# Kernel tuning notes

Measured on AMD Instinct MI355X. Metric: run time of the kernel, lower is better.

Reference implementation:

```python
import jax, jax.numpy as jnp
import numpy as np

N_NODES = 100000


def gcn_conv(x, edge_index, edge_weight, W, b):
    """PyG GCNConv: out = D^-1/2 (A + I) D^-1/2 X W + b (self-loop weight 1)."""
    n = x.shape[0]
    src, dst = edge_index[0], edge_index[1]
    loop = jnp.arange(n)
    src_sl = jnp.concatenate([src, loop])
    dst_sl = jnp.concatenate([dst, loop])
    ew_sl = jnp.concatenate([edge_weight, jnp.ones((n,), x.dtype)])
    deg = jax.ops.segment_sum(ew_sl, dst_sl, num_segments=n)  # [N]
    dinv = jnp.where(deg > 0, jax.lax.rsqrt(deg), 0.0)
    norm = dinv[src_sl] * ew_sl * dinv[dst_sl]  # [E+N]
    h = x @ W  # [N, out_dim] dense transform before propagation
    msg = h[src_sl] * norm[:, None]  # gather + scale, [E+N, out_dim]
    out = jax.ops.segment_sum(msg, dst_sl, num_segments=n)  # scatter-add
    return out + b


def setup_inputs() -> dict:
    key = jax.random.key(0)
    ks = jax.random.split(key, 9)
    in_dim, hidden, latent = 128, 64, 32
    n, e = N_NODES, 1600000
    x = jax.random.normal(ks[0], (n, in_dim), dtype=jnp.float32)
    edge_index = jax.random.randint(ks[1], (2, e), 0, n, dtype=jnp.int64)
    edge_weight = jax.random.uniform(ks[2], (e,), dtype=jnp.float32)
    def glorot(k, fan_in, fan_out):
        s = jnp.sqrt(6.0 / (fan_in + fan_out))
        return jax.random.uniform(k, (fan_in, fan_out), jnp.float32, -s, s)
    return {
        "x": x,
        "edge_index": edge_index,
        "edge_weight": edge_weight,
        "W1": glorot(ks[3], in_dim, hidden),
        "b1": jnp.zeros((hidden,), jnp.float32),
        "W_mu": glorot(ks[4], hidden, latent),
        "b_mu": jnp.zeros((latent,), jnp.float32),
        "W_lv": glorot(ks[5], hidden, latent),
        "b_lv": jnp.zeros((latent,), jnp.float32),
    }


def reference(x, edge_index, edge_weight, W1, b1, W_mu, b_mu, W_lv, b_lv):
    h = jax.nn.relu(gcn_conv(x, edge_index, edge_weight, W1, b1))
    mu = gcn_conv(h, edge_index, edge_weight, W_mu, b_mu)
    logvar = gcn_conv(h, edge_index, edge_weight, W_lv, b_lv)
    return (mu, logvar)
```

## Files before the change

### kernel.cpp

```cpp
#include <hip/hip_runtime.h>

static __device__ __forceinline__ float4 ld4(const float* p) { return *(const float4*)p; }
static __device__ __forceinline__ float b2f(unsigned short u) {
    return __uint_as_float((unsigned)u << 16);
}
static __device__ __forceinline__ float b2f_lo(unsigned u) { return __uint_as_float(u << 16); }
static __device__ __forceinline__ float b2f_hi(unsigned u) { return __uint_as_float(u & 0xFFFF0000u); }
static __device__ __forceinline__ unsigned short f2b(float f) {
    unsigned x = __float_as_uint(f);
    return (unsigned short)((x + 0x7FFFu + ((x >> 16) & 1u)) >> 16);
}
static __device__ __forceinline__ unsigned pk2(float lo, float hi) {
    return (unsigned)f2b(lo) | ((unsigned)f2b(hi) << 16);
}

#define NPB 256
#define CAPE 5120


__global__ __launch_bounds__(256) void k_fused1(const float* __restrict__ A,
                                                const float* __restrict__ W0,
                                                const float* __restrict__ dinv_unused,
                                                unsigned short* __restrict__ gout,
                                                const int* __restrict__ src,
                                                const int* __restrict__ dst,
                                                const float* __restrict__ ew,
                                                int* __restrict__ bin_cnt,
                                                unsigned long long* __restrict__ ebuf,
                                                int n, int E, int gb, int NB) {
    __shared__ float Ws[64 * 64];
    __shared__ float Xs[64 * 64];
    __shared__ int hist[512];
    __shared__ int hbase[512];
    int tid = threadIdx.x;

    if ((int)blockIdx.x < gb) {
        int row0 = blockIdx.x * 64;
        int c0 = (tid & 15) * 4;
        int r0 = (tid >> 4) * 4;
        float4 acc[4] = {};
        #pragma unroll
        for (int p = 0; p < 2; p++) {
            for (int j = tid; j < 1024; j += 256)
                *(float4*)&Ws[j * 4] = ld4(W0 + p * 4096 + j * 4);
            for (int j = tid; j < 1024; j += 256) {
                int r = j >> 4, kc = j & 15;
                int grow = row0 + r;
                float4 v = make_float4(0.f, 0.f, 0.f, 0.f);
                if (grow < n) v = ld4(A + (size_t)grow * 128 + p * 64 + kc * 4);
                *(float4*)&Xs[r * 64 + kc * 4] = v;
            }
            __syncthreads();
            #pragma unroll 4
            for (int kk = 0; kk < 64; kk += 4) {
                float4 w0 = ld4(&Ws[(kk + 0) * 64 + c0]);
                float4 w1 = ld4(&Ws[(kk + 1) * 64 + c0]);
                float4 w2 = ld4(&Ws[(kk + 2) * 64 + c0]);
                float4 w3 = ld4(&Ws[(kk + 3) * 64 + c0]);
                #pragma unroll
                for (int i = 0; i < 4; i++) {
                    float4 a = ld4(&Xs[(r0 + i) * 64 + kk]);
                    acc[i].x = fmaf(a.x, w0.x, fmaf(a.y, w1.x, fmaf(a.z, w2.x, fmaf(a.w, w3.x, acc[i].x))));
                    acc[i].y = fmaf(a.x, w0.y, fmaf(a.y, w1.y, fmaf(a.z, w2.y, fmaf(a.w, w3.y, acc[i].y))));
                    acc[i].z = fmaf(a.x, w0.z, fmaf(a.y, w1.z, fmaf(a.z, w2.z, fmaf(a.w, w3.z, acc[i].z))));
                    acc[i].w = fmaf(a.x, w0.w, fmaf(a.y, w1.w, fmaf(a.z, w2.w, fmaf(a.w, w3.w, acc[i].w))));
                }
            }
            __syncthreads();
        }
        #pragma unroll
        for (int i = 0; i < 4; i++) {
            int grow = row0 + r0 + i;
            if (grow < n) {
                ushort4 u = make_ushort4(f2b(acc[i].x), f2b(acc[i].y), f2b(acc[i].z), f2b(acc[i].w));
                *(ushort4*)&gout[(size_t)grow * 64 + c0] = u;
            }
        }
    } else {
        for (int j = tid; j < NB; j += 256) hist[j] = 0;
        __syncthreads();
        int e0 = ((int)blockIdx.x - gb) * 4096;
        unsigned long long pk[16]; int bb[16]; int loc[16];
        #pragma unroll
        for (int j = 0; j < 16; j++) {
            int e = e0 + j * 256 + tid;
            if (e < E) {
                int s = src[e];
                int d = dst[e];
                float w = ew[e];
                bb[j] = d >> 8;
                pk[j] = ((unsigned long long)__float_as_uint(w) << 32) |
                        (unsigned)((d & (NPB - 1)) << 17) | (unsigned)s;
                loc[j] = atomicAdd(&hist[bb[j]], 1);
            } else bb[j] = -1;
        }
        __syncthreads();
        for (int j = tid; j < NB; j += 256) hbase[j] = atomicAdd(&bin_cnt[j], hist[j]);
        __syncthreads();
        #pragma unroll
        for (int j = 0; j < 16; j++) {
            if (bb[j] >= 0)
                ebuf[(size_t)bb[j] * CAPE + hbase[bb[j]] + loc[j]] = pk[j];
        }
    }
}

__global__ __launch_bounds__(512) void k_csr_build(const unsigned long long* __restrict__ ebuf,
                                                   const int* __restrict__ bin_cnt,
                                                   int2* __restrict__ rowcnt,
                                                   float* __restrict__ dinv,
                                                   unsigned long long* __restrict__ csr,
                                                   int n) {
    __shared__ unsigned long long eL[CAPE];
    __shared__ unsigned cntL[NPB];
    __shared__ unsigned ewsL[NPB];
    __shared__ unsigned fillL[NPB];
    __shared__ int scanL[512];
    __shared__ int rowL[NPB];
    __shared__ int binbase_s;
    int b = blockIdx.x;
    int tid = threadIdx.x;
    if (tid < NPB) { cntL[tid] = 0; ewsL[tid] = 0; fillL[tid] = 0; }
    scanL[tid] = (tid < b) ? bin_cnt[tid] : 0;
    __syncthreads();
    int m = bin_cnt[b];
    const unsigned long long* eb = ebuf + (size_t)b * CAPE;
    for (int i = tid; i < m; i += 512) {
        unsigned long long pk = eb[i];
        eL[i] = pk;
        int ld = (int)((pk >> 17) & (NPB - 1));
        float w = __uint_as_float((unsigned)(pk >> 32));
        atomicAdd(&cntL[ld], 1u);
        atomicAdd(&ewsL[ld], (unsigned)(w * 16777216.0f));
    }
    __syncthreads();
    #pragma unroll
    for (int off = 256; off > 0; off >>= 1) {
        if (tid < off) scanL[tid] += scanL[tid + off];
        __syncthreads();
    }
    if (tid == 0) binbase_s = scanL[0];
    __syncthreads();
    int v = (tid < NPB) ? (int)cntL[tid] : 0;
    scanL[tid] = v;
    __syncthreads();
    #pragma unroll
    for (int off = 1; off < 512; off <<= 1) {
        int t = (tid >= off) ? scanL[tid - off] : 0;
        __syncthreads();
        scanL[tid] += t;
        __syncthreads();
    }
    if (tid < NPB) {
        int rp = binbase_s + scanL[tid] - v;
        rowL[tid] = rp;
        int node = b * NPB + tid;
        if (node < n) {
            rowcnt[node] = make_int2(rp, v);
            dinv[node] = rsqrtf(1.0f + (float)ewsL[tid] * (1.0f / 16777216.0f));
        }
    }
    __syncthreads();
    for (int i = tid; i < m; i += 512) {
        unsigned long long pk = eL[i];
        int s = (int)(pk & 0x1FFFF);
        int ld = (int)((pk >> 17) & (NPB - 1));
        int pos = rowL[ld] + (int)atomicAdd(&fillL[ld], 1u);
        csr[pos] = (unsigned long long)(unsigned)s | (pk & 0xFFFFFFFF00000000ull);
    }
}

__global__ __launch_bounds__(256) void k_scale(unsigned short* __restrict__ h0,
                                               const float* __restrict__ dinv, int n) {
    int i = blockIdx.x * 256 + threadIdx.x;
    if (i >= n * 16) return;
    int node = i >> 4;
    float sc = dinv[node];
    ushort4 u = *(ushort4*)&h0[(size_t)i * 4];
    u = make_ushort4(f2b(b2f(u.x) * sc), f2b(b2f(u.y) * sc),
                     f2b(b2f(u.z) * sc), f2b(b2f(u.w) * sc));
    *(ushort4*)&h0[(size_t)i * 4] = u;
}

template<int K, bool SPLITW, bool ABF16>
__global__ __launch_bounds__(256) void k_gemm(const void* __restrict__ Av,
                                              const float* __restrict__ W0,
                                              const float* __restrict__ W1s,
                                              const float* __restrict__ dinv,
                                              unsigned short* __restrict__ out, int n) {
    __shared__ float Ws[K * 64];
    __shared__ float Xs[64 * K];
    int tid = threadIdx.x;
    int row0 = blockIdx.x * 64;

    constexpr int WF4 = K * 64 / 4;
    for (int j = tid; j < WF4; j += 256) {
        float4 v;
        if (!SPLITW) {
            v = ld4(W0 + j * 4);
        } else {
            int k = (j * 4) >> 6;
            int c = (j * 4) & 63;
            v = (c < 32) ? ld4(W0 + k * 32 + c) : ld4(W1s + k * 32 + (c - 32));
        }
        *(float4*)&Ws[j * 4] = v;
    }
    constexpr int XF4PR = K / 4;
    for (int j = tid; j < 64 * XF4PR; j += 256) {
        int r = j / XF4PR, kc = j % XF4PR;
        int grow = row0 + r;
        float4 v = make_float4(0.f, 0.f, 0.f, 0.f);
        if (grow < n) {
            if (ABF16) {
                const unsigned short* Ab = (const unsigned short*)Av;
                ushort4 u = *(const ushort4*)(Ab + (size_t)grow * K + kc * 4);
                v = make_float4(b2f(u.x), b2f(u.y), b2f(u.z), b2f(u.w));
            } else {
                v = ld4((const float*)Av + (size_t)grow * K + kc * 4);
            }
        }
        *(float4*)&Xs[r * K + kc * 4] = v;
    }
    __syncthreads();

    int c0 = (tid & 15) * 4;
    int r0 = (tid >> 4) * 4;
    float4 acc[4] = {};
    #pragma unroll 4
    for (int kk = 0; kk < K; kk += 4) {
        float4 w0 = ld4(&Ws[(kk + 0) * 64 + c0]);
        float4 w1 = ld4(&Ws[(kk + 1) * 64 + c0]);
        float4 w2 = ld4(&Ws[(kk + 2) * 64 + c0]);
        float4 w3 = ld4(&Ws[(kk + 3) * 64 + c0]);
        #pragma unroll
        for (int i = 0; i < 4; i++) {
            float4 a = ld4(&Xs[(r0 + i) * K + kk]);
            acc[i].x = fmaf(a.x, w0.x, fmaf(a.y, w1.x, fmaf(a.z, w2.x, fmaf(a.w, w3.x, acc[i].x))));
            acc[i].y = fmaf(a.x, w0.y, fmaf(a.y, w1.y, fmaf(a.z, w2.y, fmaf(a.w, w3.y, acc[i].y))));
            acc[i].z = fmaf(a.x, w0.z, fmaf(a.y, w1.z, fmaf(a.z, w2.z, fmaf(a.w, w3.z, acc[i].z))));
            acc[i].w = fmaf(a.x, w0.w, fmaf(a.y, w1.w, fmaf(a.z, w2.w, fmaf(a.w, w3.w, acc[i].w))));
        }
    }
    #pragma unroll
    for (int i = 0; i < 4; i++) {
        int grow = row0 + r0 + i;
        if (grow < n) {
            float sc = dinv[grow];
            ushort4 u = make_ushort4(f2b(acc[i].x * sc), f2b(acc[i].y * sc),
                                     f2b(acc[i].z * sc), f2b(acc[i].w * sc));
            *(ushort4*)&out[(size_t)grow * 64 + c0] = u;
        }
    }
}

static __device__ __forceinline__ void acc8(float* a, uint4 r, float wt) {
    a[0] = fmaf(b2f_lo(r.x), wt, a[0]); a[1] = fmaf(b2f_hi(r.x), wt, a[1]);
    a[2] = fmaf(b2f_lo(r.y), wt, a[2]); a[3] = fmaf(b2f_hi(r.y), wt, a[3]);
    a[4] = fmaf(b2f_lo(r.z), wt, a[4]); a[5] = fmaf(b2f_hi(r.z), wt, a[5]);
    a[6] = fmaf(b2f_lo(r.w), wt, a[6]); a[7] = fmaf(b2f_hi(r.w), wt, a[7]);
}

template<bool RELU, bool SPLIT_OUT>
__global__ __launch_bounds__(256) void k_prop(const unsigned short* __restrict__ g,
                                              const int2* __restrict__ csr,
                                              const int2* __restrict__ rowcnt,
                                              const float* __restrict__ dinv,
                                              const float* __restrict__ bias0,
                                              const float* __restrict__ bias1,
                                              void* __restrict__ outv, int n) {
    int node = blockIdx.x * 4 + (threadIdx.x >> 6);
    if (node >= n) return;
    int lane = threadIdx.x & 63;
    int q = lane >> 3;
    int t = lane & 7;
    uint4 sr = *(const uint4*)(g + (size_t)node * 64 + t * 8);
    int2 rc = rowcnt[node];
    const int2* ep = csr + rc.x;
    int m = rc.y;
    float a[8] = {};
    for (int e = 0; e < m; e += 32) {
        int e1 = e + q, e2 = e1 + 8, e3 = e1 + 16, e4 = e1 + 24;
        int i1 = min(e1, m - 1), i2 = min(e2, m - 1);
        int i3 = min(e3, m - 1), i4 = min(e4, m - 1);
        int2 p1 = ep[i1];
        int2 p2 = ep[i2];
        int2 p3 = ep[i3];
        int2 p4 = ep[i4];
        uint4 r1 = *(const uint4*)(g + (size_t)p1.x * 64 + t * 8);
        uint4 r2 = *(const uint4*)(g + (size_t)p2.x * 64 + t * 8);
        uint4 r3 = *(const uint4*)(g + (size_t)p3.x * 64 + t * 8);
        uint4 r4 = *(const uint4*)(g + (size_t)p4.x * 64 + t * 8);
        float w1 = (e1 < m) ? __int_as_float(p1.y) : 0.f;
        float w2 = (e2 < m) ? __int_as_float(p2.y) : 0.f;
        float w3 = (e3 < m) ? __int_as_float(p3.y) : 0.f;
        float w4 = (e4 < m) ? __int_as_float(p4.y) : 0.f;
        acc8(a, r1, w1);
        acc8(a, r2, w2);
        acc8(a, r3, w3);
        acc8(a, r4, w4);
    }
    #pragma unroll
    for (int i = 0; i < 8; i++) {
        a[i] += __shfl_xor(a[i], 8);
        a[i] += __shfl_xor(a[i], 16);
        a[i] += __shfl_xor(a[i], 32);
    }
    if (q != 0) return;
    a[0] += b2f_lo(sr.x); a[1] += b2f_hi(sr.x);
    a[2] += b2f_lo(sr.y); a[3] += b2f_hi(sr.y);
    a[4] += b2f_lo(sr.z); a[5] += b2f_hi(sr.z);
    a[6] += b2f_lo(sr.w); a[7] += b2f_hi(sr.w);
    float di = dinv[node];
    #pragma unroll
    for (int i = 0; i < 8; i++) a[i] *= di;
    if (!SPLIT_OUT) {
        float4 b0 = ld4(bias0 + t * 8);
        float4 b1 = ld4(bias0 + t * 8 + 4);
        a[0] += b0.x; a[1] += b0.y; a[2] += b0.z; a[3] += b0.w;
        a[4] += b1.x; a[5] += b1.y; a[6] += b1.z; a[7] += b1.w;
        if (RELU) {
            #pragma unroll
            for (int i = 0; i < 8; i++) a[i] = fmaxf(a[i], 0.f);
        }
        uint4 u = make_uint4(pk2(a[0], a[1]), pk2(a[2], a[3]),
                             pk2(a[4], a[5]), pk2(a[6], a[7]));
        *(uint4*)((unsigned short*)outv + (size_t)node * 64 + t * 8) = u;
    } else {
        float* out = (float*)outv;
        const float* bp = (t < 4) ? (bias0 + t * 8) : (bias1 + (t - 4) * 8);
        size_t base = (t < 4) ? ((size_t)node * 32 + t * 8)
                              : ((size_t)n * 32 + (size_t)node * 32 + (t - 4) * 8);
        float4 b0 = ld4(bp);
        float4 b1 = ld4(bp + 4);
        float4 v0 = make_float4(a[0] + b0.x, a[1] + b0.y, a[2] + b0.z, a[3] + b0.w);
        float4 v1 = make_float4(a[4] + b1.x, a[5] + b1.y, a[6] + b1.z, a[7] + b1.w);
        *(float4*)&out[base] = v0;
        *(float4*)&out[base + 4] = v1;
    }
}

extern "C" void kernel_launch(void* const* d_in, const int* in_sizes, int n_in,
                              void* d_out, int out_size, void* d_ws, size_t ws_size,
                              hipStream_t stream) {
    const float* x   = (const float*)d_in[0];
    const int*   ei  = (const int*)d_in[1];
    const float* ew  = (const float*)d_in[2];
    const float* W1  = (const float*)d_in[3];
    const float* b1  = (const float*)d_in[4];
    const float* Wmu = (const float*)d_in[5];
    const float* bmu = (const float*)d_in[6];
    const float* Wlv = (const float*)d_in[7];
    const float* blv = (const float*)d_in[8];
    float* outp = (float*)d_out;

    const int n = in_sizes[0] / 128;
    const int E = in_sizes[2];
    const int* src = ei;
    const int* dst = ei + E;
    const int NB = (n + NPB - 1) / NPB;

    size_t o = 0;
    auto alloc = [&](size_t bytes) { void* p = (char*)d_ws + o; o += (bytes + 511) & ~(size_t)511; return p; };
    int*   bin_cnt  = (int*)alloc((size_t)NB * 4);
    int2*  rowcnt   = (int2*)alloc((size_t)n * 8);
    float* dinv     = (float*)alloc((size_t)n * 4);
    unsigned long long* csr  = (unsigned long long*)alloc((size_t)E * 8);
    unsigned long long* ebuf = (unsigned long long*)alloc((size_t)NB * CAPE * 8);
    unsigned short* g0 = (unsigned short*)alloc((size_t)n * 64 * 2);
    unsigned short* h  = (unsigned short*)alloc((size_t)n * 64 * 2);
    unsigned short* g2 = g0;

    const int gb = (n + 63) / 64;
    const int bb = (E + 4095) / 4096;

    hipMemsetAsync(bin_cnt, 0, (size_t)NB * 4, stream);
    k_fused1<<<gb + bb, 256, 0, stream>>>(x, W1, nullptr, g0, src, dst, ew,
                                          bin_cnt, ebuf, n, E, gb, NB);
    k_csr_build<<<NB, 512, 0, stream>>>(ebuf, bin_cnt, rowcnt, dinv, csr, n);
    k_scale<<<(n * 16 + 255) / 256, 256, 0, stream>>>(g0, dinv, n);
    k_prop<true, false><<<(n + 3) / 4, 256, 0, stream>>>(g0, (const int2*)csr, rowcnt, dinv,
                                                         b1, nullptr, h, n);
    k_gemm<64, true, true><<<gb, 256, 0, stream>>>(h, Wmu, Wlv, dinv, g2, n);
    k_prop<false, true><<<(n + 3) / 4, 256, 0, stream>>>(g2, (const int2*)csr, rowcnt, dinv,
                                                         bmu, blv, outp, n);
}
```

Before: 279.5 us.

## Use row-per-thread GEMMs with uniform weight loads and fold dinv scaling into CSR build

Both dense transforms are rewritten so each thread computes a full 64-wide output row in registers. Weights are read directly from global memory at uniform addresses (scalar/broadcast loads) instead of being staged in LDS tiles with barriers. The separate k_scale launch is removed: k_csr_build now keeps dinv in shared memory and rescales its bin's rows of the first-layer features in place. This saves one launch and the LDS/sync overhead, but adds heavy register pressure (64 accumulators), uncoalesced per-thread row reads, and extra work at the tail of the CSR build.

```diff
diff --git a/kernel.cpp b/kernel.cpp
--- a/kernel.cpp
+++ b/kernel.cpp
@@ -20,7 +20,6 @@
 
 __global__ __launch_bounds__(256) void k_fused1(const float* __restrict__ A,
                                                 const float* __restrict__ W0,
-                                                const float* __restrict__ dinv_unused,
                                                 unsigned short* __restrict__ gout,
                                                 const int* __restrict__ src,
                                                 const int* __restrict__ dst,
@@ -28,53 +27,46 @@
                                                 int* __restrict__ bin_cnt,
                                                 unsigned long long* __restrict__ ebuf,
                                                 int n, int E, int gb, int NB) {
-    __shared__ float Ws[64 * 64];
-    __shared__ float Xs[64 * 64];
     __shared__ int hist[512];
     __shared__ int hbase[512];
     int tid = threadIdx.x;
 
     if ((int)blockIdx.x < gb) {
-        int row0 = blockIdx.x * 64;
-        int c0 = (tid & 15) * 4;
-        int r0 = (tid >> 4) * 4;
-        float4 acc[4] = {};
-        #pragma unroll
-        for (int p = 0; p < 2; p++) {
-            for (int j = tid; j < 1024; j += 256)
-                *(float4*)&Ws[j * 4] = ld4(W0 + p * 4096 + j * 4);
-            for (int j = tid; j < 1024; j += 256) {
-                int r = j >> 4, kc = j & 15;
-                int grow = row0 + r;
-                float4 v = make_float4(0.f, 0.f, 0.f, 0.f);
-                if (grow < n) v = ld4(A + (size_t)grow * 128 + p * 64 + kc * 4);
-                *(float4*)&Xs[r * 64 + kc * 4] = v;
+        int row = blockIdx.x * 256 + tid;
+        if (row >= n) return;
+        const float* xr = A + (size_t)row * 128;
+        float acc[64];
+        #pragma unroll
+        for (int c = 0; c < 64; c++) acc[c] = 0.f;
+        float4 xa0 = ld4(xr), xa1 = ld4(xr + 4), xa2 = ld4(xr + 8), xa3 = ld4(xr + 12);
+        for (int ch = 0; ch < 8; ch++) {
+            float4 xb0, xb1, xb2, xb3;
+            bool more = (ch < 7);
+            if (more) {
+                const float* nx = xr + ch * 16 + 16;
+                xb0 = ld4(nx); xb1 = ld4(nx + 4); xb2 = ld4(nx + 8); xb3 = ld4(nx + 12);
             }
-            __syncthreads();
-            #pragma unroll 4
-            for (int kk = 0; kk < 64; kk += 4) {
-                float4 w0 = ld4(&Ws[(kk + 0) * 64 + c0]);
-                float4 w1 = ld4(&Ws[(kk + 1) * 64 + c0]);
-                float4 w2 = ld4(&Ws[(kk + 2) * 64 + c0]);
-                float4 w3 = ld4(&Ws[(kk + 3) * 64 + c0]);
+            float xs[16];
+            xs[0] = xa0.x; xs[1] = xa0.y; xs[2] = xa0.z; xs[3] = xa0.w;
+            xs[4] = xa1.x; xs[5] = xa1.y; xs[6] = xa1.z; xs[7] = xa1.w;
+            xs[8] = xa2.x; xs[9] = xa2.y; xs[10] = xa2.z; xs[11] = xa2.w;
+            xs[12] = xa3.x; xs[13] = xa3.y; xs[14] = xa3.z; xs[15] = xa3.w;
+            #pragma unroll
+            for (int kk = 0; kk < 16; kk++) {
+                float xk = xs[kk];
+                const float* wr = W0 + (size_t)(ch * 16 + kk) * 64;
                 #pragma unroll
-                for (int i = 0; i < 4; i++) {
-                    float4 a = ld4(&Xs[(r0 + i) * 64 + kk]);
-                    acc[i].x = fmaf(a.x, w0.x, fmaf(a.y, w1.x, fmaf(a.z, w2.x, fmaf(a.w, w3.x, acc[i].x))));
-                    acc[i].y = fmaf(a.x, w0.y, fmaf(a.y, w1.y, fmaf(a.z, w2.y, fmaf(a.w, w3.y, acc[i].y))));
-                    acc[i].z = fmaf(a.x, w0.z, fmaf(a.y, w1.z, fmaf(a.z, w2.z, fmaf(a.w, w3.z, acc[i].z))));
-                    acc[i].w = fmaf(a.x, w0.w, fmaf(a.y, w1.w, fmaf(a.z, w2.w, fmaf(a.w, w3.w, acc[i].w))));
-                }
+                for (int c = 0; c < 64; c++)
+                    acc[c] = fmaf(xk, wr[c], acc[c]);
             }
-            __syncthreads();
-        }
-        #pragma unroll
-        for (int i = 0; i < 4; i++) {
-            int grow = row0 + r0 + i;
-            if (grow < n) {
-                ushort4 u = make_ushort4(f2b(acc[i].x), f2b(acc[i].y), f2b(acc[i].z), f2b(acc[i].w));
-                *(ushort4*)&gout[(size_t)grow * 64 + c0] = u;
-            }
+            if (more) { xa0 = xb0; xa1 = xb1; xa2 = xb2; xa3 = xb3; }
+        }
+        unsigned short* op = gout + (size_t)row * 64;
+        #pragma unroll
+        for (int c = 0; c < 64; c += 8) {
+            uint4 u = make_uint4(pk2(acc[c], acc[c + 1]), pk2(acc[c + 2], acc[c + 3]),
+                                 pk2(acc[c + 4], acc[c + 5]), pk2(acc[c + 6], acc[c + 7]));
+            *(uint4*)(op + c) = u;
         }
     } else {
         for (int j = tid; j < NB; j += 256) hist[j] = 0;
@@ -110,6 +102,7 @@
                                                    int2* __restrict__ rowcnt,
                                                    float* __restrict__ dinv,
                                                    unsigned long long* __restrict__ csr,
+                                                   unsigned short* __restrict__ h0,
                                                    int n) {
     __shared__ unsigned long long eL[CAPE];
     __shared__ unsigned cntL[NPB];
@@ -117,6 +110,7 @@
     __shared__ unsigned fillL[NPB];
     __shared__ int scanL[512];
     __shared__ int rowL[NPB];
+    __shared__ float dinvL[NPB];
     __shared__ int binbase_s;
     int b = blockIdx.x;
     int tid = threadIdx.x;
@@ -154,10 +148,12 @@
     if (tid < NPB) {
         int rp = binbase_s + scanL[tid] - v;
         rowL[tid] = rp;
+        float dv = rsqrtf(1.0f + (float)ewsL[tid] * (1.0f / 16777216.0f));
+        dinvL[tid] = dv;
         int node = b * NPB + tid;
         if (node < n) {
             rowcnt[node] = make_int2(rp, v);
-            dinv[node] = rsqrtf(1.0f + (float)ewsL[tid] * (1.0f / 16777216.0f));
+            dinv[node] = dv;
         }
     }
     __syncthreads();
@@ -168,88 +164,76 @@
         int pos = rowL[ld] + (int)atomicAdd(&fillL[ld], 1u);
         csr[pos] = (unsigned long long)(unsigned)s | (pk & 0xFFFFFFFF00000000ull);
     }
-}
-
-__global__ __launch_bounds__(256) void k_scale(unsigned short* __restrict__ h0,
-                                               const float* __restrict__ dinv, int n) {
-    int i = blockIdx.x * 256 + threadIdx.x;
-    if (i >= n * 16) return;
-    int node = i >> 4;
-    float sc = dinv[node];
-    ushort4 u = *(ushort4*)&h0[(size_t)i * 4];
-    u = make_ushort4(f2b(b2f(u.x) * sc), f2b(b2f(u.y) * sc),
-                     f2b(b2f(u.z) * sc), f2b(b2f(u.w) * sc));
-    *(ushort4*)&h0[(size_t)i * 4] = u;
-}
-
-template<int K, bool SPLITW, bool ABF16>
-__global__ __launch_bounds__(256) void k_gemm(const void* __restrict__ Av,
-                                              const float* __restrict__ W0,
-                                              const float* __restrict__ W1s,
-                                              const float* __restrict__ dinv,
-                                              unsigned short* __restrict__ out, int n) {
-    __shared__ float Ws[K * 64];
-    __shared__ float Xs[64 * K];
-    int tid = threadIdx.x;
-    int row0 = blockIdx.x * 64;
-
-    constexpr int WF4 = K * 64 / 4;
-    for (int j = tid; j < WF4; j += 256) {
-        float4 v;
-        if (!SPLITW) {
-            v = ld4(W0 + j * 4);
-        } else {
-            int k = (j * 4) >> 6;
-            int c = (j * 4) & 63;
-            v = (c < 32) ? ld4(W0 + k * 32 + c) : ld4(W1s + k * 32 + (c - 32));
-        }
-        *(float4*)&Ws[j * 4] = v;
-    }
-    constexpr int XF4PR = K / 4;
-    for (int j = tid; j < 64 * XF4PR; j += 256) {
-        int r = j / XF4PR, kc = j % XF4PR;
-        int grow = row0 + r;
-        float4 v = make_float4(0.f, 0.f, 0.f, 0.f);
-        if (grow < n) {
-            if (ABF16) {
-                const unsigned short* Ab = (const unsigned short*)Av;
-                ushort4 u = *(const ushort4*)(Ab + (size_t)grow * K + kc * 4);
-                v = make_float4(b2f(u.x), b2f(u.y), b2f(u.z), b2f(u.w));
-            } else {
-                v = ld4((const float*)Av + (size_t)grow * K + kc * 4);
-            }
-        }
-        *(float4*)&Xs[r * K + kc * 4] = v;
-    }
-    __syncthreads();
-
-    int c0 = (tid & 15) * 4;
-    int r0 = (tid >> 4) * 4;
-    float4 acc[4] = {};
-    #pragma unroll 4
-    for (int kk = 0; kk < K; kk += 4) {
-        float4 w0 = ld4(&Ws[(kk + 0) * 64 + c0]);
-        float4 w1 = ld4(&Ws[(kk + 1) * 64 + c0]);
-        float4 w2 = ld4(&Ws[(kk + 2) * 64 + c0]);
-        float4 w3 = ld4(&Ws[(kk + 3) * 64 + c0]);
-        #pragma unroll
-        for (int i = 0; i < 4; i++) {
-            float4 a = ld4(&Xs[(r0 + i) * K + kk]);
-            acc[i].x = fmaf(a.x, w0.x, fmaf(a.y, w1.x, fmaf(a.z, w2.x, fmaf(a.w, w3.x, acc[i].x))));
-            acc[i].y = fmaf(a.x, w0.y, fmaf(a.y, w1.y, fmaf(a.z, w2.y, fmaf(a.w, w3.y, acc[i].y))));
-            acc[i].z = fmaf(a.x, w0.z, fmaf(a.y, w1.z, fmaf(a.z, w2.z, fmaf(a.w, w3.z, acc[i].z))));
-            acc[i].w = fmaf(a.x, w0.w, fmaf(a.y, w1.w, fmaf(a.z, w2.w, fmaf(a.w, w3.w, acc[i].w))));
-        }
-    }
-    #pragma unroll
-    for (int i = 0; i < 4; i++) {
-        int grow = row0 + r0 + i;
-        if (grow < n) {
-            float sc = dinv[grow];
-            ushort4 u = make_ushort4(f2b(acc[i].x * sc), f2b(acc[i].y * sc),
-                                     f2b(acc[i].z * sc), f2b(acc[i].w * sc));
-            *(ushort4*)&out[(size_t)grow * 64 + c0] = u;
-        }
+    for (int idx = tid; idx < NPB * 8; idx += 512) {
+        int ln = idx >> 3;
+        int node = b * NPB + ln;
+        if (node < n) {
+            float sc = dinvL[ln];
+            unsigned short* hp = h0 + (size_t)node * 64 + (idx & 7) * 8;
+            uint4 u = *(uint4*)hp;
+            u.x = pk2(b2f_lo(u.x) * sc, b2f_hi(u.x) * sc);
+            u.y = pk2(b2f_lo(u.y) * sc, b2f_hi(u.y) * sc);
+            u.z = pk2(b2f_lo(u.z) * sc, b2f_hi(u.z) * sc);
+            u.w = pk2(b2f_lo(u.w) * sc, b2f_hi(u.w) * sc);
+            *(uint4*)hp = u;
+        }
+    }
+}
+
+__global__ __launch_bounds__(256) void k_gemm2(const unsigned short* __restrict__ h,
+                                               const float* __restrict__ Wmu,
+                                               const float* __restrict__ Wlv,
+                                               const float* __restrict__ dinv,
+                                               unsigned short* __restrict__ out, int n) {
+    int row = blockIdx.x * 256 + threadIdx.x;
+    if (row >= n) return;
+    const unsigned short* xr = h + (size_t)row * 64;
+    float acc[64];
+    #pragma unroll
+    for (int c = 0; c < 64; c++) acc[c] = 0.f;
+    uint4 xa0 = *(const uint4*)xr;
+    uint4 xa1 = *(const uint4*)(xr + 8);
+    for (int ch = 0; ch < 4; ch++) {
+        uint4 xb0, xb1;
+        bool more = (ch < 3);
+        if (more) {
+            const unsigned short* nx = xr + ch * 16 + 16;
+            xb0 = *(const uint4*)nx;
+            xb1 = *(const uint4*)(nx + 8);
+        }
+        float xs[16];
+        xs[0] = b2f_lo(xa0.x); xs[1] = b2f_hi(xa0.x);
+        xs[2] = b2f_lo(xa0.y); xs[3] = b2f_hi(xa0.y);
+        xs[4] = b2f_lo(xa0.z); xs[5] = b2f_hi(xa0.z);
+        xs[6] = b2f_lo(xa0.w); xs[7] = b2f_hi(xa0.w);
+        xs[8] = b2f_lo(xa1.x); xs[9] = b2f_hi(xa1.x);
+        xs[10] = b2f_lo(xa1.y); xs[11] = b2f_hi(xa1.y);
+        xs[12] = b2f_lo(xa1.z); xs[13] = b2f_hi(xa1.z);
+        xs[14] = b2f_lo(xa1.w); xs[15] = b2f_hi(xa1.w);
+        #pragma unroll
+        for (int kk = 0; kk < 16; kk++) {
+            float xk = xs[kk];
+            int k = ch * 16 + kk;
+            const float* wmu = Wmu + (size_t)k * 32;
+            const float* wlv = Wlv + (size_t)k * 32;
+            #pragma unroll
+            for (int c = 0; c < 32; c++)
+                acc[c] = fmaf(xk, wmu[c], acc[c]);
+            #pragma unroll
+            for (int c = 0; c < 32; c++)
+                acc[32 + c] = fmaf(xk, wlv[c], acc[32 + c]);
+        }
+        if (more) { xa0 = xb0; xa1 = xb1; }
+    }
+    float di = dinv[row];
+    unsigned short* op = out + (size_t)row * 64;
+    #pragma unroll
+    for (int c = 0; c < 64; c += 8) {
+        uint4 u = make_uint4(pk2(acc[c] * di, acc[c + 1] * di),
+                             pk2(acc[c + 2] * di, acc[c + 3] * di),
+                             pk2(acc[c + 4] * di, acc[c + 5] * di),
+                             pk2(acc[c + 6] * di, acc[c + 7] * di));
+        *(uint4*)(op + c) = u;
     }
 }
 
@@ -370,17 +354,16 @@
     unsigned short* h  = (unsigned short*)alloc((size_t)n * 64 * 2);
     unsigned short* g2 = g0;
 
-    const int gb = (n + 63) / 64;
+    const int gb = (n + 255) / 256;
     const int bb = (E + 4095) / 4096;
 
     hipMemsetAsync(bin_cnt, 0, (size_t)NB * 4, stream);
-    k_fused1<<<gb + bb, 256, 0, stream>>>(x, W1, nullptr, g0, src, dst, ew,
+    k_fused1<<<gb + bb, 256, 0, stream>>>(x, W1, g0, src, dst, ew,
                                           bin_cnt, ebuf, n, E, gb, NB);
-    k_csr_build<<<NB, 512, 0, stream>>>(ebuf, bin_cnt, rowcnt, dinv, csr, n);
-    k_scale<<<(n * 16 + 255) / 256, 256, 0, stream>>>(g0, dinv, n);
+    k_csr_build<<<NB, 512, 0, stream>>>(ebuf, bin_cnt, rowcnt, dinv, csr, g0, n);
     k_prop<true, false><<<(n + 3) / 4, 256, 0, stream>>>(g0, (const int2*)csr, rowcnt, dinv,
                                                          b1, nullptr, h, n);
-    k_gemm<64, true, true><<<gb, 256, 0, stream>>>(h, Wmu, Wlv, dinv, g2, n);
+    k_gemm2<<<gb, 256, 0, stream>>>(h, Wmu, Wlv, dinv, g2, n);
     k_prop<false, true><<<(n + 3) / 4, 256, 0, stream>>>(g2, (const int2*)csr, rowcnt, dinv,
                                                          bmu, blv, outp, n);
 }
```

Measured after the change: 483.7 us. 73.0% more time.

## Fuse dinv scaling into CSR build and enlarge GEMM tiles to 128 rows

Applied to the files above, without the earlier changes.

Removes the separate k_scale launch. The per-node dinv scaling of the first GEMM output now happens at the end of k_csr_build, using a shared-memory copy of dinv. Both dense GEMM kernels now process 128 rows per block with 8 rows per thread, and use an XOR swizzle on the X tile in shared memory to reduce LDS bank conflicts. The second GEMM is specialised to read bf16 input with 16-byte loads. The costs are more shared memory and registers per block, and fewer GEMM blocks to overlap with the edge-binning blocks.

```diff
diff --git a/kernel.cpp b/kernel.cpp
--- a/kernel.cpp
+++ b/kernel.cpp
@@ -18,9 +18,9 @@
 #define CAPE 5120
 
 
+
 __global__ __launch_bounds__(256) void k_fused1(const float* __restrict__ A,
                                                 const float* __restrict__ W0,
-                                                const float* __restrict__ dinv_unused,
                                                 unsigned short* __restrict__ gout,
                                                 const int* __restrict__ src,
                                                 const int* __restrict__ dst,
@@ -29,37 +29,40 @@
                                                 unsigned long long* __restrict__ ebuf,
                                                 int n, int E, int gb, int NB) {
     __shared__ float Ws[64 * 64];
-    __shared__ float Xs[64 * 64];
+    __shared__ float Xs[128 * 64];
     __shared__ int hist[512];
     __shared__ int hbase[512];
     int tid = threadIdx.x;
 
     if ((int)blockIdx.x < gb) {
-        int row0 = blockIdx.x * 64;
+        int row0 = blockIdx.x * 128;
         int c0 = (tid & 15) * 4;
-        int r0 = (tid >> 4) * 4;
-        float4 acc[4] = {};
+        int rb = tid >> 4;
+        int r0 = rb * 8;
+        int swz = rb * 4;
+        float4 acc[8] = {};
         #pragma unroll
         for (int p = 0; p < 2; p++) {
             for (int j = tid; j < 1024; j += 256)
                 *(float4*)&Ws[j * 4] = ld4(W0 + p * 4096 + j * 4);
-            for (int j = tid; j < 1024; j += 256) {
-                int r = j >> 4, kc = j & 15;
+            for (int j = tid; j < 2048; j += 256) {
+                int r = j >> 4, kc = (j & 15) * 4;
                 int grow = row0 + r;
                 float4 v = make_float4(0.f, 0.f, 0.f, 0.f);
-                if (grow < n) v = ld4(A + (size_t)grow * 128 + p * 64 + kc * 4);
-                *(float4*)&Xs[r * 64 + kc * 4] = v;
+                if (grow < n) v = ld4(A + (size_t)grow * 128 + p * 64 + kc);
+                int sw = ((r >> 3) & 15) * 4;
+                *(float4*)&Xs[r * 64 + (kc ^ sw)] = v;
             }
             __syncthreads();
-            #pragma unroll 4
+            #pragma unroll 2
             for (int kk = 0; kk < 64; kk += 4) {
                 float4 w0 = ld4(&Ws[(kk + 0) * 64 + c0]);
                 float4 w1 = ld4(&Ws[(kk + 1) * 64 + c0]);
                 float4 w2 = ld4(&Ws[(kk + 2) * 64 + c0]);
                 float4 w3 = ld4(&Ws[(kk + 3) * 64 + c0]);
                 #pragma unroll
-                for (int i = 0; i < 4; i++) {
-                    float4 a = ld4(&Xs[(r0 + i) * 64 + kk]);
+                for (int i = 0; i < 8; i++) {
+                    float4 a = ld4(&Xs[(r0 + i) * 64 + (kk ^ swz)]);
                     acc[i].x = fmaf(a.x, w0.x, fmaf(a.y, w1.x, fmaf(a.z, w2.x, fmaf(a.w, w3.x, acc[i].x))));
                     acc[i].y = fmaf(a.x, w0.y, fmaf(a.y, w1.y, fmaf(a.z, w2.y, fmaf(a.w, w3.y, acc[i].y))));
                     acc[i].z = fmaf(a.x, w0.z, fmaf(a.y, w1.z, fmaf(a.z, w2.z, fmaf(a.w, w3.z, acc[i].z))));
@@ -69,7 +72,7 @@
             __syncthreads();
         }
         #pragma unroll
-        for (int i = 0; i < 4; i++) {
+        for (int i = 0; i < 8; i++) {
             int grow = row0 + r0 + i;
             if (grow < n) {
                 ushort4 u = make_ushort4(f2b(acc[i].x), f2b(acc[i].y), f2b(acc[i].z), f2b(acc[i].w));
@@ -110,6 +113,7 @@
                                                    int2* __restrict__ rowcnt,
                                                    float* __restrict__ dinv,
                                                    unsigned long long* __restrict__ csr,
+                                                   unsigned short* __restrict__ h0,
                                                    int n) {
     __shared__ unsigned long long eL[CAPE];
     __shared__ unsigned cntL[NPB];
@@ -117,6 +121,7 @@
     __shared__ unsigned fillL[NPB];
     __shared__ int scanL[512];
     __shared__ int rowL[NPB];
+    __shared__ float dinvL[NPB];
     __shared__ int binbase_s;
     int b = blockIdx.x;
     int tid = threadIdx.x;
@@ -154,10 +159,12 @@
     if (tid < NPB) {
         int rp = binbase_s + scanL[tid] - v;
         rowL[tid] = rp;
+        float dv = rsqrtf(1.0f + (float)ewsL[tid] * (1.0f / 16777216.0f));
+        dinvL[tid] = dv;
         int node = b * NPB + tid;
         if (node < n) {
             rowcnt[node] = make_int2(rp, v);
-            dinv[node] = rsqrtf(1.0f + (float)ewsL[tid] * (1.0f / 16777216.0f));
+            dinv[node] = dv;
         }
     }
     __syncthreads();
@@ -168,73 +175,64 @@
         int pos = rowL[ld] + (int)atomicAdd(&fillL[ld], 1u);
         csr[pos] = (unsigned long long)(unsigned)s | (pk & 0xFFFFFFFF00000000ull);
     }
-}
-
-__global__ __launch_bounds__(256) void k_scale(unsigned short* __restrict__ h0,
-                                               const float* __restrict__ dinv, int n) {
-    int i = blockIdx.x * 256 + threadIdx.x;
-    if (i >= n * 16) return;
-    int node = i >> 4;
-    float sc = dinv[node];
-    ushort4 u = *(ushort4*)&h0[(size_t)i * 4];
-    u = make_ushort4(f2b(b2f(u.x) * sc), f2b(b2f(u.y) * sc),
-                     f2b(b2f(u.z) * sc), f2b(b2f(u.w) * sc));
-    *(ushort4*)&h0[(size_t)i * 4] = u;
-}
-
-template<int K, bool SPLITW, bool ABF16>
-__global__ __launch_bounds__(256) void k_gemm(const void* __restrict__ Av,
-                                              const float* __restrict__ W0,
-                                              const float* __restrict__ W1s,
-                                              const float* __restrict__ dinv,
-                                              unsigned short* __restrict__ out, int n) {
-    __shared__ float Ws[K * 64];
-    __shared__ float Xs[64 * K];
+    for (int idx = tid; idx < NPB * 8; idx += 512) {
+        int ln = idx >> 3;
+        int node = b * NPB + ln;
+        if (node < n) {
+            float sc = dinvL[ln];
+            unsigned short* hp = h0 + (size_t)node * 64 + (idx & 7) * 8;
+            uint4 u = *(uint4*)hp;
+            u.x = pk2(b2f_lo(u.x) * sc, b2f_hi(u.x) * sc);
+            u.y = pk2(b2f_lo(u.y) * sc, b2f_hi(u.y) * sc);
+            u.z = pk2(b2f_lo(u.z) * sc, b2f_hi(u.z) * sc);
+            u.w = pk2(b2f_lo(u.w) * sc, b2f_hi(u.w) * sc);
+            *(uint4*)hp = u;
+        }
+    }
+}
+
+__global__ __launch_bounds__(256) void k_gemm2(const unsigned short* __restrict__ h,
+                                               const float* __restrict__ Wmu,
+                                               const float* __restrict__ Wlv,
+                                               const float* __restrict__ dinv,
+                                               unsigned short* __restrict__ out, int n) {
+    __shared__ float Ws[64 * 64];
+    __shared__ float Xs[128 * 64];
     int tid = threadIdx.x;
-    int row0 = blockIdx.x * 64;
-
-    constexpr int WF4 = K * 64 / 4;
-    for (int j = tid; j < WF4; j += 256) {
-        float4 v;
-        if (!SPLITW) {
-            v = ld4(W0 + j * 4);
-        } else {
-            int k = (j * 4) >> 6;
-            int c = (j * 4) & 63;
-            v = (c < 32) ? ld4(W0 + k * 32 + c) : ld4(W1s + k * 32 + (c - 32));
-        }
+    int row0 = blockIdx.x * 128;
+    for (int j = tid; j < 1024; j += 256) {
+        int k = (j * 4) >> 6;
+        int c = (j * 4) & 63;
+        float4 v = (c < 32) ? ld4(Wmu + k * 32 + c) : ld4(Wlv + k * 32 + (c - 32));
         *(float4*)&Ws[j * 4] = v;
     }
-    constexpr int XF4PR = K / 4;
-    for (int j = tid; j < 64 * XF4PR; j += 256) {
-        int r = j / XF4PR, kc = j % XF4PR;
+    for (int j = tid; j < 1024; j += 256) {
+        int r = j >> 3, ko = (j & 7) * 8;
         int grow = row0 + r;
-        float4 v = make_float4(0.f, 0.f, 0.f, 0.f);
-        if (grow < n) {
-            if (ABF16) {
-                const unsigned short* Ab = (const unsigned short*)Av;
-                ushort4 u = *(const ushort4*)(Ab + (size_t)grow * K + kc * 4);
-                v = make_float4(b2f(u.x), b2f(u.y), b2f(u.z), b2f(u.w));
-            } else {
-                v = ld4((const float*)Av + (size_t)grow * K + kc * 4);
-            }
-        }
-        *(float4*)&Xs[r * K + kc * 4] = v;
+        uint4 u = make_uint4(0u, 0u, 0u, 0u);
+        if (grow < n) u = *(const uint4*)(h + (size_t)grow * 64 + ko);
+        int sw = ((r >> 3) & 15) * 4;
+        float4 v0 = make_float4(b2f_lo(u.x), b2f_hi(u.x), b2f_lo(u.y), b2f_hi(u.y));
+        float4 v1 = make_float4(b2f_lo(u.z), b2f_hi(u.z), b2f_lo(u.w), b2f_hi(u.w));
+        *(float4*)&Xs[r * 64 + (ko ^ sw)] = v0;
+        *(float4*)&Xs[r * 64 + ((ko + 4) ^ sw)] = v1;
     }
     __syncthreads();
 
     int c0 = (tid & 15) * 4;
-    int r0 = (tid >> 4) * 4;
-    float4 acc[4] = {};
-    #pragma unroll 4
-    for (int kk = 0; kk < K; kk += 4) {
+    int rb = tid >> 4;
+    int r0 = rb * 8;
+    int swz = rb * 4;
+    float4 acc[8] = {};
+    #pragma unroll 2
+    for (int kk = 0; kk < 64; kk += 4) {
         float4 w0 = ld4(&Ws[(kk + 0) * 64 + c0]);
         float4 w1 = ld4(&Ws[(kk + 1) * 64 + c0]);
         float4 w2 = ld4(&Ws[(kk + 2) * 64 + c0]);
         float4 w3 = ld4(&Ws[(kk + 3) * 64 + c0]);
         #pragma unroll
-        for (int i = 0; i < 4; i++) {
-            float4 a = ld4(&Xs[(r0 + i) * K + kk]);
+        for (int i = 0; i < 8; i++) {
+            float4 a = ld4(&Xs[(r0 + i) * 64 + (kk ^ swz)]);
             acc[i].x = fmaf(a.x, w0.x, fmaf(a.y, w1.x, fmaf(a.z, w2.x, fmaf(a.w, w3.x, acc[i].x))));
             acc[i].y = fmaf(a.x, w0.y, fmaf(a.y, w1.y, fmaf(a.z, w2.y, fmaf(a.w, w3.y, acc[i].y))));
             acc[i].z = fmaf(a.x, w0.z, fmaf(a.y, w1.z, fmaf(a.z, w2.z, fmaf(a.w, w3.z, acc[i].z))));
@@ -242,7 +240,7 @@
         }
     }
     #pragma unroll
-    for (int i = 0; i < 4; i++) {
+    for (int i = 0; i < 8; i++) {
         int grow = row0 + r0 + i;
         if (grow < n) {
             float sc = dinv[grow];
@@ -370,17 +368,16 @@
     unsigned short* h  = (unsigned short*)alloc((size_t)n * 64 * 2);
     unsigned short* g2 = g0;
 
-    const int gb = (n + 63) / 64;
+    const int gb = (n + 127) / 128;
     const int bb = (E + 4095) / 4096;
 
     hipMemsetAsync(bin_cnt, 0, (size_t)NB * 4, stream);
-    k_fused1<<<gb + bb, 256, 0, stream>>>(x, W1, nullptr, g0, src, dst, ew,
+    k_fused1<<<gb + bb, 256, 0, stream>>>(x, W1, g0, src, dst, ew,
                                           bin_cnt, ebuf, n, E, gb, NB);
-    k_csr_build<<<NB, 512, 0, stream>>>(ebuf, bin_cnt, rowcnt, dinv, csr, n);
-    k_scale<<<(n * 16 + 255) / 256, 256, 0, stream>>>(g0, dinv, n);
+    k_csr_build<<<NB, 512, 0, stream>>>(ebuf, bin_cnt, rowcnt, dinv, csr, g0, n);
     k_prop<true, false><<<(n + 3) / 4, 256, 0, stream>>>(g0, (const int2*)csr, rowcnt, dinv,
                                                          b1, nullptr, h, n);
-    k_gemm<64, true, true><<<gb, 256, 0, stream>>>(h, Wmu, Wlv, dinv, g2, n);
+    k_gemm2<<<gb, 256, 0, stream>>>(h, Wmu, Wlv, dinv, g2, n);
     k_prop<false, true><<<(n + 3) / 4, 256, 0, stream>>>(g2, (const int2*)csr, rowcnt, dinv,
                                                          bmu, blv, outp, n);
 }
```

New measurement: 277.7 us. Within noise of the previous version (-0.6%).
